# Kernel tuning notes

Measured on AMD Instinct MI355X. Metric: run time of the kernel, lower is better.

The kernel has to match this reference:

```python
import jax, jax.numpy as jnp
import numpy as np

H = 2048            # hidden_size
INTER = 8192        # intermediate_size
E = 16              # num_experts
V = 32000           # vocab_size
I = INTER // E      # per-expert intermediate (tp_size=1) = 512
N = 4096            # num_tokens
BASE_ROUTING_SCALE = 10.0


def setup_inputs() -> dict:
    key = jax.random.key(0)
    ks = jax.random.split(key, 6)
    x = jax.random.normal(ks[0], (N, H), dtype=jnp.float32)
    token_ids = jax.random.randint(ks[1], (N,), 0, V)
    mu = jax.random.normal(ks[2], (N, H), dtype=jnp.float32)
    # kaiming-uniform-ish scaled params
    gate_up_proj = jax.random.normal(ks[3], (E, H, 2 * I), dtype=jnp.float32) * (1.0 / np.sqrt(H))
    down_proj = jax.random.normal(ks[4], (E, I, H), dtype=jnp.float32) * (1.0 / np.sqrt(I))
    # mu_router initialized to zeros in the module; use small random so routing is actually mu-biased
    mu_router_w = jax.random.normal(ks[5], (E, H), dtype=jnp.float32) * 0.02
    return {"x": x, "token_ids": token_ids, "mu": mu,
            "gate_up_proj": gate_up_proj, "down_proj": down_proj,
            "mu_router_w": mu_router_w}


def reference(x, token_ids, mu, gate_up_proj, down_proj, mu_router_w):
    # --- routing: expert = token_id % E, biased by mu logits ---
    base = jnp.clip(token_ids, 0, V - 1) % E              # [N]
    logits = (jax.nn.one_hot(base, E, dtype=jnp.float32) * BASE_ROUTING_SCALE
              + mu @ mu_router_w.T)                       # [N, E]
    expert_ids = jnp.argmax(logits, axis=-1)              # [N]

    Iloc = gate_up_proj.shape[-1] // 2

    # --- grouped expert SwiGLU MLP: scan over experts, mask-combine outputs ---
    def step(acc, inp):
        wg, wd, e = inp
        gu = x @ wg                                       # [N, 2I]
        h = jax.nn.silu(gu[:, :Iloc]) * gu[:, Iloc:]      # [N, I]
        o = h @ wd                                        # [N, H]
        acc = acc + jnp.where((expert_ids == e)[:, None], o, 0.0)
        return acc, None

    out0 = jnp.zeros_like(x)
    out, _ = jax.lax.scan(step, out0, (gate_up_proj, down_proj, jnp.arange(E)))
    return out
```

## Files before the change

kernel.cpp:

```cpp
#include <hip/hip_runtime.h>
#include <hip/hip_bf16.h>

#define NT 4096
#define HD 2048
#define NE 16
#define ID 512
#define TWO_I 1024
#define LP 266
#define MAXITEMS 47

typedef __attribute__((ext_vector_type(8))) short bf16x8_t;
typedef __attribute__((ext_vector_type(4))) float f32x4_t;

__device__ __forceinline__ unsigned short f2bf(float f) {
  union { float f; unsigned int u; } v; v.f = f;
  unsigned int r = v.u + 0x7fffu + ((v.u >> 16) & 1u);
  return (unsigned short)(r >> 16);
}
__device__ __forceinline__ unsigned pk2(unsigned short a, unsigned short b) {
  return (unsigned)a | ((unsigned)b << 16);
}
__device__ __forceinline__ void gl_lds16(const void* g, void* l) {
  __builtin_amdgcn_global_load_lds(
      (const __attribute__((address_space(1))) unsigned int*)g,
      (__attribute__((address_space(3))) unsigned int*)l, 16, 0, 0);
}

__global__ __launch_bounds__(256) void k_prep_gu(const float* __restrict__ gup,
                                                 unsigned short* __restrict__ wgb) {
  int kt = blockIdx.x, e = blockIdx.y;
  int K0 = kt * 64;
  int t = threadIdx.x, w = t >> 6, lane = t & 63;
  __shared__ unsigned short L[64 * LP];
  int cgrp = t >> 3, m = t & 7;
  int kc = m ^ (cgrp & 7);
  for (int q = 0; q < 4; ++q) {
    for (int rd = 0; rd < 16; ++rd) {
      int row = rd * 4 + w;
      const float* s = gup + ((size_t)e * HD + K0 + row) * TWO_I + q * 256 + lane * 4;
      float4 v = *(const float4*)s;
      uint2 p; p.x = pk2(f2bf(v.x), f2bf(v.y)); p.y = pk2(f2bf(v.z), f2bf(v.w));
      *(uint2*)&L[row * LP + lane * 4] = p;
    }
    __syncthreads();
#pragma unroll
    for (int it = 0; it < 8; ++it) {
      int Cl = it * 32 + cgrp;
      int cb = q * 4 + (Cl >> 6), c = Cl & 63;
      const unsigned short* src = &L[(kc * 8) * LP + Cl];
      unsigned short tv[8];
#pragma unroll
      for (int j = 0; j < 8; ++j) tv[j] = src[j * LP];
      uint4 val;
      val.x = pk2(tv[0], tv[1]); val.y = pk2(tv[2], tv[3]);
      val.z = pk2(tv[4], tv[5]); val.w = pk2(tv[6], tv[7]);
      unsigned short* dst = wgb + (((size_t)e * 16 + cb) * 32 + kt) * 4096 + c * 64 + m * 8;
      *(uint4*)dst = val;
    }
    __syncthreads();
  }
}
__global__ __launch_bounds__(256) void k_prep_dn(const float* __restrict__ dwn,
                                                 unsigned short* __restrict__ wdb) {
  int kt = blockIdx.x, e = blockIdx.y, half = blockIdx.z;
  int K0 = kt * 64;
  int t = threadIdx.x, w = t >> 6, lane = t & 63;
  __shared__ unsigned short L[64 * LP];
  int cgrp = t >> 3, m = t & 7;
  int kc = m ^ (cgrp & 7);
  for (int q = 0; q < 4; ++q) {
    for (int rd = 0; rd < 16; ++rd) {
      int row = rd * 4 + w;
      const float* s = dwn + ((size_t)e * ID + K0 + row) * HD + half * 1024 + q * 256 + lane * 4;
      float4 v = *(const float4*)s;
      uint2 p; p.x = pk2(f2bf(v.x), f2bf(v.y)); p.y = pk2(f2bf(v.z), f2bf(v.w));
      *(uint2*)&L[row * LP + lane * 4] = p;
    }
    __syncthreads();
#pragma unroll
    for (int it = 0; it < 8; ++it) {
      int Cl = it * 32 + cgrp;
      int cb = half * 16 + q * 4 + (Cl >> 6), c = Cl & 63;
      const unsigned short* src = &L[(kc * 8) * LP + Cl];
      unsigned short tv[8];
#pragma unroll
      for (int j = 0; j < 8; ++j) tv[j] = src[j * LP];
      uint4 val;
      val.x = pk2(tv[0], tv[1]); val.y = pk2(tv[2], tv[3]);
      val.z = pk2(tv[4], tv[5]); val.w = pk2(tv[6], tv[7]);
      unsigned short* dst = wdb + (((size_t)e * 32 + cb) * 8 + kt) * 4096 + c * 64 + m * 8;
      *(uint4*)dst = val;
    }
    __syncthreads();
  }
}

__global__ void k_cast_x(const float* __restrict__ x, unsigned short* __restrict__ xb) {
  size_t i = ((size_t)blockIdx.x * 256 + threadIdx.x) * 8;
  float4 a = *(const float4*)(x + i);
  float4 b = *(const float4*)(x + i + 4);
  uint4 pk;
  pk.x = pk2(f2bf(a.x), f2bf(a.y)); pk.y = pk2(f2bf(a.z), f2bf(a.w));
  pk.z = pk2(f2bf(b.x), f2bf(b.y)); pk.w = pk2(f2bf(b.z), f2bf(b.w));
  *(uint4*)(xb + i) = pk;
}

__global__ void k_route(const float* __restrict__ mu, const int* __restrict__ tok,
                        const float* __restrict__ wr, int* __restrict__ eid) {
  int t = blockIdx.x;
  int tid = threadIdx.x;
  float p[NE];
#pragma unroll
  for (int e = 0; e < NE; ++e) p[e] = 0.f;
  const float* m = mu + (size_t)t * HD;
  for (int h = tid; h < HD; h += 256) {
    float mv = m[h];
#pragma unroll
    for (int e = 0; e < NE; ++e) p[e] += mv * wr[e * HD + h];
  }
#pragma unroll
  for (int e = 0; e < NE; ++e) {
    float v = p[e];
#pragma unroll
    for (int s = 32; s; s >>= 1) v += __shfl_xor(v, s, 64);
    p[e] = v;
  }
  __shared__ float red[4][NE];
  int lane = tid & 63, wv = tid >> 6;
  if (lane == 0) {
#pragma unroll
    for (int e = 0; e < NE; ++e) red[wv][e] = p[e];
  }
  __syncthreads();
  if (tid == 0) {
    int tk = tok[t];
    if (tk < 0) tk = 0;
    if (tk > 31999) tk = 31999;
    int base = tk & 15;
    float best = -3.0e38f; int bi = 0;
    for (int e = 0; e < NE; ++e) {
      float v = red[0][e] + red[1][e] + red[2][e] + red[3][e];
      if (e == base) v += 10.0f;
      if (v > best) { best = v; bi = e; }
    }
    eid[t] = bi;
  }
}

__global__ void k_init(int* counts, int* cursors) {
  int i = threadIdx.x;
  if (i < NE) { counts[i] = 0; cursors[i] = 0; }
}
__global__ void k_hist(const int* __restrict__ eid, int* __restrict__ counts) {
  int t = blockIdx.x * 256 + threadIdx.x;
  if (t < NT) atomicAdd(&counts[eid[t]], 1);
}
__global__ void k_scan(const int* __restrict__ counts, int* __restrict__ offsets,
                       int* __restrict__ cursors, int* __restrict__ wk) {
  if (threadIdx.x == 0) {
    int s = 0;
    for (int e = 0; e < NE; ++e) { offsets[e] = s; cursors[e] = s; s += counts[e]; }
    offsets[NE] = s;
    int n = 0;
    for (int e = 0; e < NE; ++e) {
      int tiles = (counts[e] + 127) >> 7;
      for (int m = 0; m < tiles; ++m) { wk[n++] = e | (m << 8); }
    }
    wk[MAXITEMS] = n;
  }
}
__global__ void k_scatter(const int* __restrict__ eid, int* __restrict__ cursors,
                          int* __restrict__ tlist) {
  int t = blockIdx.x * 256 + threadIdx.x;
  if (t < NT) {
    int e = eid[t];
    int pos = atomicAdd(&cursors[e], 1);
    tlist[pos] = t;
  }
}

__global__ __launch_bounds__(256, 2) void k_gemm1(
    const unsigned short* __restrict__ xb, const unsigned short* __restrict__ wgb,
    const int* __restrict__ offsets, const int* __restrict__ tlist,
    const int* __restrict__ wk, unsigned short* __restrict__ hbuf) {
  int item = blockIdx.y;
  if (item >= wk[MAXITEMS]) return;
  int w = wk[item];
  int e = w & 255, tb = (w >> 8) * 128;
  int off = offsets[e], cnt = offsets[e + 1] - off;
  int cx = blockIdx.x;
  int c0 = cx * 64;

  __shared__ unsigned short Pb[4][2][4096];
  __shared__ int ltok[128];

  int tid = threadIdx.x, lane = tid & 63, wv = tid >> 6;
  if (tid < 128) { int r = tb + tid; if (r > cnt - 1) r = cnt - 1; ltok[tid] = tlist[off + r]; }
  __syncthreads();

  int lr = lane & 15, hi = lane >> 4, mb = wv * 32;
  const unsigned short* aRow0 = xb + (size_t)ltok[mb + lr] * HD + hi * 8;
  const unsigned short* aRow1 = xb + (size_t)ltok[mb + 16 + lr] * HD + hi * 8;

  int gu = wv >> 1, part = wv & 1;
  const unsigned short* wS =
      wgb + (((size_t)e * 16 + (gu ? 8 + cx : cx)) * 32) * 4096 + part * 2048 + lane * 8;

#define STAGEB(BUF) do { \
  gl_lds16(wS,        &Pb[BUF][gu][part * 2048]); \
  gl_lds16(wS + 512,  &Pb[BUF][gu][part * 2048 + 512]); \
  gl_lds16(wS + 1024, &Pb[BUF][gu][part * 2048 + 1024]); \
  gl_lds16(wS + 1536, &Pb[BUF][gu][part * 2048 + 1536]); \
  wS += 4096; } while (0)

  bf16x8_t A0[4], A1[4], A2[4], A3[4];
#define LOADA(SET, KT) do { \
  SET[0] = *(const bf16x8_t*)(aRow0 + (KT) * 64); \
  SET[1] = *(const bf16x8_t*)(aRow0 + (KT) * 64 + 32); \
  SET[2] = *(const bf16x8_t*)(aRow1 + (KT) * 64); \
  SET[3] = *(const bf16x8_t*)(aRow1 + (KT) * 64 + 32); } while (0)

  f32x4_t zero = {0.f, 0.f, 0.f, 0.f};
  f32x4_t accg[2][4], accu[2][4];
#pragma unroll
  for (int m = 0; m < 2; ++m)
#pragma unroll
    for (int n = 0; n < 4; ++n) { accg[m][n] = zero; accu[m][n] = zero; }

#define MFMA_PH(BUF, SET) do { \
  __builtin_amdgcn_s_setprio(1); \
  _Pragma("unroll") for (int kk = 0; kk < 2; ++kk) { \
    int cidx = kk * 4 + hi; \
    bf16x8_t a0 = SET[kk], a1 = SET[2 + kk]; \
    _Pragma("unroll") for (int n = 0; n < 4; ++n) { \
      int r = n * 16 + lr; \
      int o = r * 64 + ((cidx ^ (r & 7)) * 8); \
      bf16x8_t bg = *(bf16x8_t*)&Pb[BUF][0][o]; \
      bf16x8_t bu = *(bf16x8_t*)&Pb[BUF][1][o]; \
      accg[0][n] = __builtin_amdgcn_mfma_f32_16x16x32_bf16(a0, bg, accg[0][n], 0, 0, 0); \
      accu[0][n] = __builtin_amdgcn_mfma_f32_16x16x32_bf16(a0, bu, accu[0][n], 0, 0, 0); \
      accg[1][n] = __builtin_amdgcn_mfma_f32_16x16x32_bf16(a1, bg, accg[1][n], 0, 0, 0); \
      accu[1][n] = __builtin_amdgcn_mfma_f32_16x16x32_bf16(a1, bu, accu[1][n], 0, 0, 0); \
    } } \
  __builtin_amdgcn_s_setprio(0); } while (0)

#define SUBSTEP(KT, BUF, SETC, SETN, VMC) do { \
  asm volatile("s_waitcnt vmcnt(" #VMC ")" ::: "memory"); \
  __builtin_amdgcn_sched_barrier(0); \
  __builtin_amdgcn_s_barrier(); \
  MFMA_PH(BUF, SETC); \
  if ((KT) + 3 < 32) { LOADA(SETN, (KT) + 3); STAGEB(((BUF) + 3) & 3); } \
} while (0)

  LOADA(A0, 0); STAGEB(0);
  LOADA(A1, 1); STAGEB(1);
  LOADA(A2, 2); STAGEB(2);

  for (int g = 0; g < 7; ++g) {
    int k4 = g * 4;
    SUBSTEP(k4 + 0, 0, A0, A3, 16);
    SUBSTEP(k4 + 1, 1, A1, A0, 16);
    SUBSTEP(k4 + 2, 2, A2, A1, 16);
    SUBSTEP(k4 + 3, 3, A3, A2, 16);
  }
  SUBSTEP(28, 0, A0, A3, 16);
  SUBSTEP(29, 1, A1, A0, 16);
  SUBSTEP(30, 2, A2, A1, 8);
  SUBSTEP(31, 3, A3, A2, 0);

#undef SUBSTEP
#undef MFMA_PH
#undef LOADA
#undef STAGEB

  int rq = hi * 4;
#pragma unroll
  for (int m = 0; m < 2; ++m)
#pragma unroll
    for (int n = 0; n < 4; ++n)
#pragma unroll
      for (int j = 0; j < 4; ++j) {
        int r = tb + mb + m * 16 + rq + j;
        if (r < cnt) {
          float g = accg[m][n][j], u = accu[m][n][j];
          float hv = (g / (1.f + __expf(-g))) * u;
          hbuf[(size_t)(off + r) * ID + c0 + n * 16 + lr] = f2bf(hv);
        }
      }
}

__global__ __launch_bounds__(256, 2) void k_gemm2(
    const unsigned short* __restrict__ hbuf, const unsigned short* __restrict__ wdb,
    const int* __restrict__ offsets, const int* __restrict__ tlist,
    const int* __restrict__ wk, float* __restrict__ out) {
  int item = blockIdx.y;
  if (item >= wk[MAXITEMS]) return;
  int w = wk[item];
  int e = w & 255, tb = (w >> 8) * 128;
  int off = offsets[e], cnt = offsets[e + 1] - off;
  int cx = blockIdx.x;
  int c0 = cx * 128;

  __shared__ unsigned short Pb[4][2][4096];

  int tid = threadIdx.x, lane = tid & 63, wv = tid >> 6;
  int lr = lane & 15, hi = lane >> 4, mb = wv * 32;

  int r0 = tb + mb + lr;      if (r0 > cnt - 1) r0 = cnt - 1;
  int r1 = tb + mb + 16 + lr; if (r1 > cnt - 1) r1 = cnt - 1;
  const unsigned short* aRow0 = hbuf + (size_t)(off + r0) * ID + hi * 8;
  const unsigned short* aRow1 = hbuf + (size_t)(off + r1) * ID + hi * 8;

  int gu = wv >> 1, part = wv & 1;
  const unsigned short* wS =
      wdb + (((size_t)e * 32 + 2 * cx + gu) * 8) * 4096 + part * 2048 + lane * 8;

#define STAGEB(BUF) do { \
  gl_lds16(wS,        &Pb[BUF][gu][part * 2048]); \
  gl_lds16(wS + 512,  &Pb[BUF][gu][part * 2048 + 512]); \
  gl_lds16(wS + 1024, &Pb[BUF][gu][part * 2048 + 1024]); \
  gl_lds16(wS + 1536, &Pb[BUF][gu][part * 2048 + 1536]); \
  wS += 4096; } while (0)

  bf16x8_t A0[4], A1[4], A2[4], A3[4];
#define LOADA(SET, KT) do { \
  SET[0] = *(const bf16x8_t*)(aRow0 + (KT) * 64); \
  SET[1] = *(const bf16x8_t*)(aRow0 + (KT) * 64 + 32); \
  SET[2] = *(const bf16x8_t*)(aRow1 + (KT) * 64); \
  SET[3] = *(const bf16x8_t*)(aRow1 + (KT) * 64 + 32); } while (0)

  f32x4_t zero = {0.f, 0.f, 0.f, 0.f};
  f32x4_t acc[2][8];
#pragma unroll
  for (int m = 0; m < 2; ++m)
#pragma unroll
    for (int n = 0; n < 8; ++n) acc[m][n] = zero;

#define MFMA_PH(BUF, SET) do { \
  __builtin_amdgcn_s_setprio(1); \
  _Pragma("unroll") for (int kk = 0; kk < 2; ++kk) { \
    int cidx = kk * 4 + hi; \
    bf16x8_t a0 = SET[kk], a1 = SET[2 + kk]; \
    _Pragma("unroll") for (int n = 0; n < 8; ++n) { \
      int r = (n & 3) * 16 + lr; \
      int o = r * 64 + ((cidx ^ (r & 7)) * 8); \
      bf16x8_t b = *(bf16x8_t*)&Pb[BUF][n >> 2][o]; \
      acc[0][n] = __builtin_amdgcn_mfma_f32_16x16x32_bf16(a0, b, acc[0][n], 0, 0, 0); \
      acc[1][n] = __builtin_amdgcn_mfma_f32_16x16x32_bf16(a1, b, acc[1][n], 0, 0, 0); \
    } } \
  __builtin_amdgcn_s_setprio(0); } while (0)

#define SUBSTEP(KT, BUF, SETC, SETN, VMC) do { \
  asm volatile("s_waitcnt vmcnt(" #VMC ")" ::: "memory"); \
  __builtin_amdgcn_sched_barrier(0); \
  __builtin_amdgcn_s_barrier(); \
  MFMA_PH(BUF, SETC); \
  if ((KT) + 3 < 8) { LOADA(SETN, (KT) + 3); STAGEB(((BUF) + 3) & 3); } \
} while (0)

  LOADA(A0, 0); STAGEB(0);
  LOADA(A1, 1); STAGEB(1);
  LOADA(A2, 2); STAGEB(2);

  SUBSTEP(0, 0, A0, A3, 16);
  SUBSTEP(1, 1, A1, A0, 16);
  SUBSTEP(2, 2, A2, A1, 16);
  SUBSTEP(3, 3, A3, A2, 16);
  SUBSTEP(4, 0, A0, A3, 16);
  SUBSTEP(5, 1, A1, A0, 16);
  SUBSTEP(6, 2, A2, A1, 8);
  SUBSTEP(7, 3, A3, A2, 0);

#undef SUBSTEP
#undef MFMA_PH
#undef LOADA
#undef STAGEB

  int rq = hi * 4;
#pragma unroll
  for (int m = 0; m < 2; ++m)
#pragma unroll
    for (int n = 0; n < 8; ++n)
#pragma unroll
      for (int j = 0; j < 4; ++j) {
        int r = tb + mb + m * 16 + rq + j;
        if (r < cnt) {
          out[(size_t)tlist[off + r] * HD + c0 + n * 16 + lr] = acc[m][n][j];
        }
      }
}

extern "C" void kernel_launch(void* const* d_in, const int* in_sizes, int n_in,
                              void* d_out, int out_size, void* d_ws, size_t ws_size,
                              hipStream_t stream) {
  (void)in_sizes; (void)n_in; (void)out_size; (void)ws_size;
  const float* x   = (const float*)d_in[0];
  const int*   tok = (const int*)d_in[1];
  const float* mu  = (const float*)d_in[2];
  const float* gup = (const float*)d_in[3];
  const float* dwn = (const float*)d_in[4];
  const float* wr  = (const float*)d_in[5];
  float* out = (float*)d_out;

  char* ws = (char*)d_ws;
  int* eid     = (int*)ws;
  int* tlist   = (int*)(ws + 16384);
  int* counts  = (int*)(ws + 32768);
  int* offsets = (int*)(ws + 32896);
  int* cursors = (int*)(ws + 33024);
  int* wk      = (int*)(ws + 33152);
  unsigned short* xb   = (unsigned short*)(ws + 65536);
  unsigned short* hbuf = (unsigned short*)(ws + 65536 + 16777216);
  unsigned short* wgb  = (unsigned short*)(ws + 65536 + 16777216 + 4194304);
  unsigned short* wdb  = (unsigned short*)(ws + 65536 + 16777216 + 4194304 + 67108864);

  k_prep_gu<<<dim3(32, 16), 256, 0, stream>>>(gup, wgb);
  k_prep_dn<<<dim3(8, 16, 2), 256, 0, stream>>>(dwn, wdb);
  k_cast_x <<<4096, 256, 0, stream>>>(x, xb);
  k_route  <<<NT, 256, 0, stream>>>(mu, tok, wr, eid);
  k_init   <<<1, 64, 0, stream>>>(counts, cursors);
  k_hist   <<<16, 256, 0, stream>>>(eid, counts);
  k_scan   <<<1, 64, 0, stream>>>(counts, offsets, cursors, wk);
  k_scatter<<<16, 256, 0, stream>>>(eid, cursors, tlist);
  k_gemm1  <<<dim3(8, MAXITEMS), 256, 0, stream>>>(xb, wgb, offsets, tlist, wk, hbuf);
  k_gemm2  <<<dim3(16, MAXITEMS), 256, 0, stream>>>(hbuf, wdb, offsets, tlist, wk, out);
}
```

Baseline: 221.6 us.

## Use 256-row tiles with LDS-staged A operand in both expert GEMMs

Both grouped GEMMs switch from 128-token tiles with A loaded straight into registers to 256-token tiles on 512-thread blocks. A and B are both staged through a triple-buffered LDS pipeline using global_load_lds, and the 8 waves form a 4x2 grid so each B tile is reused across more rows. The histogram kernel is folded into routing via an atomic per token. The aim is less redundant weight traffic and fewer launches, at the cost of more LDS per block (about 120 KB), likely lower occupancy, and more padding waste on partially filled expert tiles.

```diff
diff --git a/kernel.cpp b/kernel.cpp
--- a/kernel.cpp
+++ b/kernel.cpp
@@ -7,7 +7,7 @@
 #define ID 512
 #define TWO_I 1024
 #define LP 266
-#define MAXITEMS 47
+#define MAXIT 31
 
 typedef __attribute__((ext_vector_type(8))) short bf16x8_t;
 typedef __attribute__((ext_vector_type(4))) float f32x4_t;
@@ -106,7 +106,8 @@
 }
 
 __global__ void k_route(const float* __restrict__ mu, const int* __restrict__ tok,
-                        const float* __restrict__ wr, int* __restrict__ eid) {
+                        const float* __restrict__ wr, int* __restrict__ eid,
+                        int* __restrict__ counts) {
   int t = blockIdx.x;
   int tid = threadIdx.x;
   float p[NE];
@@ -144,16 +145,13 @@
       if (v > best) { best = v; bi = e; }
     }
     eid[t] = bi;
+    atomicAdd(&counts[bi], 1);
   }
 }
 
 __global__ void k_init(int* counts, int* cursors) {
   int i = threadIdx.x;
   if (i < NE) { counts[i] = 0; cursors[i] = 0; }
-}
-__global__ void k_hist(const int* __restrict__ eid, int* __restrict__ counts) {
-  int t = blockIdx.x * 256 + threadIdx.x;
-  if (t < NT) atomicAdd(&counts[eid[t]], 1);
 }
 __global__ void k_scan(const int* __restrict__ counts, int* __restrict__ offsets,
                        int* __restrict__ cursors, int* __restrict__ wk) {
@@ -163,10 +161,10 @@
     offsets[NE] = s;
     int n = 0;
     for (int e = 0; e < NE; ++e) {
-      int tiles = (counts[e] + 127) >> 7;
+      int tiles = (counts[e] + 255) >> 8;
       for (int m = 0; m < tiles; ++m) { wk[n++] = e | (m << 8); }
     }
-    wk[MAXITEMS] = n;
+    wk[MAXIT] = n;
   }
 }
 __global__ void k_scatter(const int* __restrict__ eid, int* __restrict__ cursors,
@@ -179,213 +177,207 @@
   }
 }
 
-__global__ __launch_bounds__(256, 2) void k_gemm1(
+__global__ __launch_bounds__(512, 2) void k_gemm1(
     const unsigned short* __restrict__ xb, const unsigned short* __restrict__ wgb,
     const int* __restrict__ offsets, const int* __restrict__ tlist,
     const int* __restrict__ wk, unsigned short* __restrict__ hbuf) {
   int item = blockIdx.y;
-  if (item >= wk[MAXITEMS]) return;
+  if (item >= wk[MAXIT]) return;
   int w = wk[item];
-  int e = w & 255, tb = (w >> 8) * 128;
+  int e = w & 255, tb = (w >> 8) * 256;
   int off = offsets[e], cnt = offsets[e + 1] - off;
   int cx = blockIdx.x;
   int c0 = cx * 64;
 
-  __shared__ unsigned short Pb[4][2][4096];
-  __shared__ int ltok[128];
+  __shared__ unsigned short Ab[3][256 * 64];
+  __shared__ unsigned short Bb[3][2][4096];
+  __shared__ int ltok[256];
 
   int tid = threadIdx.x, lane = tid & 63, wv = tid >> 6;
-  if (tid < 128) { int r = tb + tid; if (r > cnt - 1) r = cnt - 1; ltok[tid] = tlist[off + r]; }
+  if (tid < 256) { int r = tb + tid; if (r > cnt - 1) r = cnt - 1; ltok[tid] = tlist[off + r]; }
   __syncthreads();
 
-  int lr = lane & 15, hi = lane >> 4, mb = wv * 32;
-  const unsigned short* aRow0 = xb + (size_t)ltok[mb + lr] * HD + hi * 8;
-  const unsigned short* aRow1 = xb + (size_t)ltok[mb + 16 + lr] * HD + hi * 8;
-
-  int gu = wv >> 1, part = wv & 1;
-  const unsigned short* wS =
-      wgb + (((size_t)e * 16 + (gu ? 8 + cx : cx)) * 32) * 4096 + part * 2048 + lane * 8;
-
-#define STAGEB(BUF) do { \
-  gl_lds16(wS,        &Pb[BUF][gu][part * 2048]); \
-  gl_lds16(wS + 512,  &Pb[BUF][gu][part * 2048 + 512]); \
-  gl_lds16(wS + 1024, &Pb[BUF][gu][part * 2048 + 1024]); \
-  gl_lds16(wS + 1536, &Pb[BUF][gu][part * 2048 + 1536]); \
-  wS += 4096; } while (0)
-
-  bf16x8_t A0[4], A1[4], A2[4], A3[4];
-#define LOADA(SET, KT) do { \
-  SET[0] = *(const bf16x8_t*)(aRow0 + (KT) * 64); \
-  SET[1] = *(const bf16x8_t*)(aRow0 + (KT) * 64 + 32); \
-  SET[2] = *(const bf16x8_t*)(aRow1 + (KT) * 64); \
-  SET[3] = *(const bf16x8_t*)(aRow1 + (KT) * 64 + 32); } while (0)
+  int lr = lane & 15, hi = lane >> 4;
+  int wr = wv >> 1, wc = wv & 1;
+
+  const unsigned short* aS[4];
+  int aD[4];
+  int cswz = (lane & 7) ^ ((lane >> 3) & 7);
+#pragma unroll
+  for (int i = 0; i < 4; ++i) {
+    int row = wv * 32 + i * 8 + (lane >> 3);
+    aS[i] = xb + (size_t)ltok[row] * HD + cswz * 8;
+    aD[i] = (wv * 32 + i * 8) * 64;
+  }
+  int bgu = wv >> 2, bpart = wv & 3;
+  const unsigned short* bS =
+      wgb + (((size_t)e * 16 + (bgu ? 8 + cx : cx)) * 32) * 4096 + bpart * 1024 + lane * 8;
+  int bD = bpart * 1024;
+
+#define STAGE(BUF) do { \
+  _Pragma("unroll") for (int i = 0; i < 4; ++i) { gl_lds16(aS[i], &Ab[BUF][aD[i]]); aS[i] += 64; } \
+  gl_lds16(bS, &Bb[BUF][bgu][bD]); gl_lds16(bS + 512, &Bb[BUF][bgu][bD + 512]); \
+  bS += 4096; } while (0)
 
   f32x4_t zero = {0.f, 0.f, 0.f, 0.f};
-  f32x4_t accg[2][4], accu[2][4];
-#pragma unroll
-  for (int m = 0; m < 2; ++m)
-#pragma unroll
-    for (int n = 0; n < 4; ++n) { accg[m][n] = zero; accu[m][n] = zero; }
-
-#define MFMA_PH(BUF, SET) do { \
-  __builtin_amdgcn_s_setprio(1); \
-  _Pragma("unroll") for (int kk = 0; kk < 2; ++kk) { \
-    int cidx = kk * 4 + hi; \
-    bf16x8_t a0 = SET[kk], a1 = SET[2 + kk]; \
-    _Pragma("unroll") for (int n = 0; n < 4; ++n) { \
-      int r = n * 16 + lr; \
-      int o = r * 64 + ((cidx ^ (r & 7)) * 8); \
-      bf16x8_t bg = *(bf16x8_t*)&Pb[BUF][0][o]; \
-      bf16x8_t bu = *(bf16x8_t*)&Pb[BUF][1][o]; \
-      accg[0][n] = __builtin_amdgcn_mfma_f32_16x16x32_bf16(a0, bg, accg[0][n], 0, 0, 0); \
-      accu[0][n] = __builtin_amdgcn_mfma_f32_16x16x32_bf16(a0, bu, accu[0][n], 0, 0, 0); \
-      accg[1][n] = __builtin_amdgcn_mfma_f32_16x16x32_bf16(a1, bg, accg[1][n], 0, 0, 0); \
-      accu[1][n] = __builtin_amdgcn_mfma_f32_16x16x32_bf16(a1, bu, accu[1][n], 0, 0, 0); \
-    } } \
-  __builtin_amdgcn_s_setprio(0); } while (0)
-
-#define SUBSTEP(KT, BUF, SETC, SETN, VMC) do { \
+  f32x4_t accg[4][2], accu[4][2];
+#pragma unroll
+  for (int m = 0; m < 4; ++m)
+#pragma unroll
+    for (int n = 0; n < 2; ++n) { accg[m][n] = zero; accu[m][n] = zero; }
+
+#define SUBSTEP(KT, BUF, VMC) do { \
   asm volatile("s_waitcnt vmcnt(" #VMC ")" ::: "memory"); \
   __builtin_amdgcn_sched_barrier(0); \
   __builtin_amdgcn_s_barrier(); \
-  MFMA_PH(BUF, SETC); \
-  if ((KT) + 3 < 32) { LOADA(SETN, (KT) + 3); STAGEB(((BUF) + 3) & 3); } \
+  bf16x8_t A_[2][4], Bg_[2][2], Bu_[2][2]; \
+  _Pragma("unroll") for (int kk = 0; kk < 2; ++kk) { \
+    int ch = kk * 4 + hi; \
+    _Pragma("unroll") for (int m = 0; m < 4; ++m) { \
+      int R = wr * 64 + m * 16 + lr; \
+      A_[kk][m] = *(bf16x8_t*)&Ab[BUF][R * 64 + ((ch ^ (R & 7)) * 8)]; } \
+    _Pragma("unroll") for (int n = 0; n < 2; ++n) { \
+      int C = wc * 32 + n * 16 + lr; \
+      int o = C * 64 + ((ch ^ (C & 7)) * 8); \
+      Bg_[kk][n] = *(bf16x8_t*)&Bb[BUF][0][o]; \
+      Bu_[kk][n] = *(bf16x8_t*)&Bb[BUF][1][o]; } } \
+  asm volatile("s_waitcnt lgkmcnt(0)" ::: "memory"); \
+  __builtin_amdgcn_sched_barrier(0); \
+  __builtin_amdgcn_s_barrier(); \
+  __builtin_amdgcn_s_setprio(1); \
+  _Pragma("unroll") for (int kk = 0; kk < 2; ++kk) \
+    _Pragma("unroll") for (int m = 0; m < 4; ++m) \
+      _Pragma("unroll") for (int n = 0; n < 2; ++n) { \
+        accg[m][n] = __builtin_amdgcn_mfma_f32_16x16x32_bf16(A_[kk][m], Bg_[kk][n], accg[m][n], 0, 0, 0); \
+        accu[m][n] = __builtin_amdgcn_mfma_f32_16x16x32_bf16(A_[kk][m], Bu_[kk][n], accu[m][n], 0, 0, 0); } \
+  __builtin_amdgcn_s_setprio(0); \
+  if ((KT) + 3 < 32) STAGE(BUF); \
 } while (0)
 
-  LOADA(A0, 0); STAGEB(0);
-  LOADA(A1, 1); STAGEB(1);
-  LOADA(A2, 2); STAGEB(2);
-
-  for (int g = 0; g < 7; ++g) {
-    int k4 = g * 4;
-    SUBSTEP(k4 + 0, 0, A0, A3, 16);
-    SUBSTEP(k4 + 1, 1, A1, A0, 16);
-    SUBSTEP(k4 + 2, 2, A2, A1, 16);
-    SUBSTEP(k4 + 3, 3, A3, A2, 16);
-  }
-  SUBSTEP(28, 0, A0, A3, 16);
-  SUBSTEP(29, 1, A1, A0, 16);
-  SUBSTEP(30, 2, A2, A1, 8);
-  SUBSTEP(31, 3, A3, A2, 0);
+  STAGE(0); STAGE(1); STAGE(2);
+
+  for (int g3 = 0; g3 < 10; ++g3) {
+    SUBSTEP(g3 * 3 + 0, 0, 12);
+    SUBSTEP(g3 * 3 + 1, 1, 12);
+    SUBSTEP(g3 * 3 + 2, 2, 12);
+  }
+  SUBSTEP(30, 0, 6);
+  SUBSTEP(31, 1, 0);
 
 #undef SUBSTEP
-#undef MFMA_PH
-#undef LOADA
-#undef STAGEB
+#undef STAGE
 
   int rq = hi * 4;
 #pragma unroll
-  for (int m = 0; m < 2; ++m)
-#pragma unroll
-    for (int n = 0; n < 4; ++n)
+  for (int m = 0; m < 4; ++m)
+#pragma unroll
+    for (int n = 0; n < 2; ++n)
 #pragma unroll
       for (int j = 0; j < 4; ++j) {
-        int r = tb + mb + m * 16 + rq + j;
+        int r = tb + wr * 64 + m * 16 + rq + j;
         if (r < cnt) {
           float g = accg[m][n][j], u = accu[m][n][j];
           float hv = (g / (1.f + __expf(-g))) * u;
-          hbuf[(size_t)(off + r) * ID + c0 + n * 16 + lr] = f2bf(hv);
+          hbuf[(size_t)(off + r) * ID + c0 + wc * 32 + n * 16 + lr] = f2bf(hv);
         }
       }
 }
 
-__global__ __launch_bounds__(256, 2) void k_gemm2(
+__global__ __launch_bounds__(512, 2) void k_gemm2(
     const unsigned short* __restrict__ hbuf, const unsigned short* __restrict__ wdb,
     const int* __restrict__ offsets, const int* __restrict__ tlist,
     const int* __restrict__ wk, float* __restrict__ out) {
   int item = blockIdx.y;
-  if (item >= wk[MAXITEMS]) return;
+  if (item >= wk[MAXIT]) return;
   int w = wk[item];
-  int e = w & 255, tb = (w >> 8) * 128;
+  int e = w & 255, tb = (w >> 8) * 256;
   int off = offsets[e], cnt = offsets[e + 1] - off;
   int cx = blockIdx.x;
   int c0 = cx * 128;
 
-  __shared__ unsigned short Pb[4][2][4096];
+  __shared__ unsigned short Ab[3][256 * 64];
+  __shared__ unsigned short Bb[3][2][4096];
 
   int tid = threadIdx.x, lane = tid & 63, wv = tid >> 6;
-  int lr = lane & 15, hi = lane >> 4, mb = wv * 32;
-
-  int r0 = tb + mb + lr;      if (r0 > cnt - 1) r0 = cnt - 1;
-  int r1 = tb + mb + 16 + lr; if (r1 > cnt - 1) r1 = cnt - 1;
-  const unsigned short* aRow0 = hbuf + (size_t)(off + r0) * ID + hi * 8;
-  const unsigned short* aRow1 = hbuf + (size_t)(off + r1) * ID + hi * 8;
-
-  int gu = wv >> 1, part = wv & 1;
-  const unsigned short* wS =
-      wdb + (((size_t)e * 32 + 2 * cx + gu) * 8) * 4096 + part * 2048 + lane * 8;
-
-#define STAGEB(BUF) do { \
-  gl_lds16(wS,        &Pb[BUF][gu][part * 2048]); \
-  gl_lds16(wS + 512,  &Pb[BUF][gu][part * 2048 + 512]); \
-  gl_lds16(wS + 1024, &Pb[BUF][gu][part * 2048 + 1024]); \
-  gl_lds16(wS + 1536, &Pb[BUF][gu][part * 2048 + 1536]); \
-  wS += 4096; } while (0)
-
-  bf16x8_t A0[4], A1[4], A2[4], A3[4];
-#define LOADA(SET, KT) do { \
-  SET[0] = *(const bf16x8_t*)(aRow0 + (KT) * 64); \
-  SET[1] = *(const bf16x8_t*)(aRow0 + (KT) * 64 + 32); \
-  SET[2] = *(const bf16x8_t*)(aRow1 + (KT) * 64); \
-  SET[3] = *(const bf16x8_t*)(aRow1 + (KT) * 64 + 32); } while (0)
+  int lr = lane & 15, hi = lane >> 4;
+  int wr = wv >> 1, wc = wv & 1;
+
+  const unsigned short* aS[4];
+  int aD[4];
+  int cswz = (lane & 7) ^ ((lane >> 3) & 7);
+#pragma unroll
+  for (int i = 0; i < 4; ++i) {
+    int r = tb + wv * 32 + i * 8 + (lane >> 3);
+    if (r > cnt - 1) r = cnt - 1;
+    aS[i] = hbuf + (size_t)(off + r) * ID + cswz * 8;
+    aD[i] = (wv * 32 + i * 8) * 64;
+  }
+  int bgu = wv >> 2, bpart = wv & 3;
+  const unsigned short* bS =
+      wdb + (((size_t)e * 32 + 2 * cx + bgu) * 8) * 4096 + bpart * 1024 + lane * 8;
+  int bD = bpart * 1024;
+
+#define STAGE(BUF) do { \
+  _Pragma("unroll") for (int i = 0; i < 4; ++i) { gl_lds16(aS[i], &Ab[BUF][aD[i]]); aS[i] += 64; } \
+  gl_lds16(bS, &Bb[BUF][bgu][bD]); gl_lds16(bS + 512, &Bb[BUF][bgu][bD + 512]); \
+  bS += 4096; } while (0)
 
   f32x4_t zero = {0.f, 0.f, 0.f, 0.f};
-  f32x4_t acc[2][8];
-#pragma unroll
-  for (int m = 0; m < 2; ++m)
-#pragma unroll
-    for (int n = 0; n < 8; ++n) acc[m][n] = zero;
-
-#define MFMA_PH(BUF, SET) do { \
-  __builtin_amdgcn_s_setprio(1); \
-  _Pragma("unroll") for (int kk = 0; kk < 2; ++kk) { \
-    int cidx = kk * 4 + hi; \
-    bf16x8_t a0 = SET[kk], a1 = SET[2 + kk]; \
-    _Pragma("unroll") for (int n = 0; n < 8; ++n) { \
-      int r = (n & 3) * 16 + lr; \
-      int o = r * 64 + ((cidx ^ (r & 7)) * 8); \
-      bf16x8_t b = *(bf16x8_t*)&Pb[BUF][n >> 2][o]; \
-      acc[0][n] = __builtin_amdgcn_mfma_f32_16x16x32_bf16(a0, b, acc[0][n], 0, 0, 0); \
-      acc[1][n] = __builtin_amdgcn_mfma_f32_16x16x32_bf16(a1, b, acc[1][n], 0, 0, 0); \
-    } } \
-  __builtin_amdgcn_s_setprio(0); } while (0)
-
-#define SUBSTEP(KT, BUF, SETC, SETN, VMC) do { \
+  f32x4_t acc[4][4];
+#pragma unroll
+  for (int m = 0; m < 4; ++m)
+#pragma unroll
+    for (int n = 0; n < 4; ++n) acc[m][n] = zero;
+
+#define SUBSTEP(KT, BUF, VMC) do { \
   asm volatile("s_waitcnt vmcnt(" #VMC ")" ::: "memory"); \
   __builtin_amdgcn_sched_barrier(0); \
   __builtin_amdgcn_s_barrier(); \
-  MFMA_PH(BUF, SETC); \
-  if ((KT) + 3 < 8) { LOADA(SETN, (KT) + 3); STAGEB(((BUF) + 3) & 3); } \
+  bf16x8_t A_[2][4], B_[2][4]; \
+  _Pragma("unroll") for (int kk = 0; kk < 2; ++kk) { \
+    int ch = kk * 4 + hi; \
+    _Pragma("unroll") for (int m = 0; m < 4; ++m) { \
+      int R = wr * 64 + m * 16 + lr; \
+      A_[kk][m] = *(bf16x8_t*)&Ab[BUF][R * 64 + ((ch ^ (R & 7)) * 8)]; } \
+    _Pragma("unroll") for (int n = 0; n < 4; ++n) { \
+      int C = n * 16 + lr; \
+      B_[kk][n] = *(bf16x8_t*)&Bb[BUF][wc][C * 64 + ((ch ^ (C & 7)) * 8)]; } } \
+  asm volatile("s_waitcnt lgkmcnt(0)" ::: "memory"); \
+  __builtin_amdgcn_sched_barrier(0); \
+  __builtin_amdgcn_s_barrier(); \
+  __builtin_amdgcn_s_setprio(1); \
+  _Pragma("unroll") for (int kk = 0; kk < 2; ++kk) \
+    _Pragma("unroll") for (int m = 0; m < 4; ++m) \
+      _Pragma("unroll") for (int n = 0; n < 4; ++n) \
+        acc[m][n] = __builtin_amdgcn_mfma_f32_16x16x32_bf16(A_[kk][m], B_[kk][n], acc[m][n], 0, 0, 0); \
+  __builtin_amdgcn_s_setprio(0); \
+  if ((KT) + 3 < 8) STAGE(BUF); \
 } while (0)
 
-  LOADA(A0, 0); STAGEB(0);
-  LOADA(A1, 1); STAGEB(1);
-  LOADA(A2, 2); STAGEB(2);
-
-  SUBSTEP(0, 0, A0, A3, 16);
-  SUBSTEP(1, 1, A1, A0, 16);
-  SUBSTEP(2, 2, A2, A1, 16);
-  SUBSTEP(3, 3, A3, A2, 16);
-  SUBSTEP(4, 0, A0, A3, 16);
-  SUBSTEP(5, 1, A1, A0, 16);
-  SUBSTEP(6, 2, A2, A1, 8);
-  SUBSTEP(7, 3, A3, A2, 0);
+  STAGE(0); STAGE(1); STAGE(2);
+
+  SUBSTEP(0, 0, 12);
+  SUBSTEP(1, 1, 12);
+  SUBSTEP(2, 2, 12);
+  SUBSTEP(3, 0, 12);
+  SUBSTEP(4, 1, 12);
+  SUBSTEP(5, 2, 12);
+  SUBSTEP(6, 0, 6);
+  SUBSTEP(7, 1, 0);
 
 #undef SUBSTEP
-#undef MFMA_PH
-#undef LOADA
-#undef STAGEB
+#undef STAGE
 
   int rq = hi * 4;
 #pragma unroll
-  for (int m = 0; m < 2; ++m)
-#pragma unroll
-    for (int n = 0; n < 8; ++n)
+  for (int m = 0; m < 4; ++m)
+#pragma unroll
+    for (int n = 0; n < 4; ++n)
 #pragma unroll
       for (int j = 0; j < 4; ++j) {
-        int r = tb + mb + m * 16 + rq + j;
+        int r = tb + wr * 64 + m * 16 + rq + j;
         if (r < cnt) {
-          out[(size_t)tlist[off + r] * HD + c0 + n * 16 + lr] = acc[m][n][j];
+          out[(size_t)tlist[off + r] * HD + c0 + wc * 64 + n * 16 + lr] = acc[m][n][j];
         }
       }
 }
@@ -417,11 +409,10 @@
   k_prep_gu<<<dim3(32, 16), 256, 0, stream>>>(gup, wgb);
   k_prep_dn<<<dim3(8, 16, 2), 256, 0, stream>>>(dwn, wdb);
   k_cast_x <<<4096, 256, 0, stream>>>(x, xb);
-  k_route  <<<NT, 256, 0, stream>>>(mu, tok, wr, eid);
   k_init   <<<1, 64, 0, stream>>>(counts, cursors);
-  k_hist   <<<16, 256, 0, stream>>>(eid, counts);
+  k_route  <<<NT, 256, 0, stream>>>(mu, tok, wr, eid, counts);
   k_scan   <<<1, 64, 0, stream>>>(counts, offsets, cursors, wk);
   k_scatter<<<16, 256, 0, stream>>>(eid, cursors, tlist);
-  k_gemm1  <<<dim3(8, MAXITEMS), 256, 0, stream>>>(xb, wgb, offsets, tlist, wk, hbuf);
-  k_gemm2  <<<dim3(16, MAXITEMS), 256, 0, stream>>>(hbuf, wdb, offsets, tlist, wk, out);
-}
+  k_gemm1  <<<dim3(8, MAXIT), 512, 0, stream>>>(xb, wgb, offsets, tlist, wk, hbuf);
+  k_gemm2  <<<dim3(16, MAXIT), 512, 0, stream>>>(hbuf, wdb, offsets, tlist, wk, out);
+}
```

New measurement: 246.8 us. 1.11x slower.
